# Kernel optimization log

Hardware: AMD Instinct MI355X
Metric: run time of the kernel (lower is better)

The kernel has to match this reference:

```python
import jax, jax.numpy as jnp
import numpy as np

MAX_STEPS = 8
EPS = 0.1
LAM = 5.0


def setup_inputs() -> dict:
    key = jax.random.key(0)
    k1, k2, k3, k4, k5 = jax.random.split(key, 5)
    n0 = m0 = 192
    E = 191  # tree edges ~ n0 - 1
    return {
        "E1f": jax.random.randint(k1, (E, 2), 0, n0),
        "E1b": jax.random.randint(k2, (E, 2), 0, n0),
        "E2f": jax.random.randint(k3, (E, 2), 0, n0),  # unused by forward (kept for signature parity)
        "cost": jax.random.uniform(k4, (n0, m0), dtype=jnp.float32),
        "constr_f": jax.random.uniform(k5, (m0, m0), dtype=jnp.float32),
    }


def reference(E1f, E1b, E2f, cost, constr_f):
    n0, m0 = cost.shape
    S = n0 + m0
    # pad cost -> [S, S], constr_f -> [S, S] (right cols zero then bottom rows one)
    cost_p = jnp.pad(cost, ((0, m0), (0, n0)))
    cf = jnp.pad(constr_f, ((0, 0), (0, n0)))
    cf = jnp.pad(cf, ((0, n0), (0, 0)), constant_values=1.0)

    phi = cost_p.T                          # [S, S]
    phie = phi / EPS
    psi_f = (LAM * (1.0 - cf))[:, :, None]  # [S, S, 1]
    psi_b = jnp.transpose(psi_f, (1, 0, 2))

    # cdist(dst, arange(S)) == 0 indicator is exactly a one-hot of the dst index
    to_f = jax.nn.one_hot(E1f[:, 1], S, dtype=phi.dtype)  # [E, S]
    to_b = jax.nn.one_hot(E1b[:, 1], S, dtype=phi.dtype)  # [E, S]
    E = to_f.shape[0]

    def step(carry, _):
        u, v, msg_f, msg_b, sum_f, sum_b = carry
        base = sum_f + sum_b - phie
        u = jax.nn.logsumexp(base - v, axis=-2, keepdims=True)  # [1, S]
        v = jax.nn.logsumexp(base - u, axis=-1, keepdims=True)  # [S, 1]
        A = phie + u + v - sum_f - sum_b                        # [S, S]
        term_f = A @ to_f.T                                     # [S, E]
        lse_f = jax.nn.logsumexp(-(psi_f / EPS + msg_b[:, None, :]), axis=0)  # [S, E]
        msg_f = 0.5 * (msg_f + term_f + lse_f)
        sum_f = msg_f @ to_f                                    # [S, S]
        A2 = phie + u + v - sum_f - sum_b
        term_b = A2 @ to_b.T
        lse_b = jax.nn.logsumexp(-(psi_b / EPS + msg_f[:, None, :]), axis=0)
        msg_b = 0.5 * (msg_b + term_b + lse_b)
        sum_b = msg_b @ to_b
        return (u, v, msg_f, msg_b, sum_f, sum_b), None

    f32 = phi.dtype
    init = (
        jnp.zeros((1, S), f32), jnp.zeros((S, 1), f32),
        jnp.zeros((S, E), f32), jnp.zeros((S, E), f32),
        jnp.zeros((S, S), f32), jnp.zeros((S, S), f32),
    )
    (u, v, _, _, sum_f, sum_b), _ = jax.lax.scan(step, init, None, length=MAX_STEPS)

    logp = jnp.minimum(sum_f + sum_b - phie - u - v, 0.0)
    return jnp.exp(logp).T
```

## Files before the change

### kernel.cpp

```cpp
#include <hip/hip_runtime.h>
#include <math.h>

#define S      384
#define N0     192
#define NE     191
#define MAXADJ 16
#define E50    1.9287498e-22f

#define OFF_W     0
#define OFF_WT    36864
#define OFF_PHIE  73728
#define OFF_MSGF  147456
#define OFF_MSGB  221184
#define OFF_MXF   294912
#define OFF_MXB   368640
#define OFF_SBT   442368
#define OFF_BASET 516096
#define OFF_U     589824
#define OFF_V     590016
#define OFF_MAXF  590400
#define OFF_MAXB  590592
#define OFF_HIF   590784
#define OFF_LOF   590976
#define OFF_HIB   591168
#define OFF_LOB   591360
#define OFF_UHI   591552
#define OFF_INT   591616
#define IOFF_DSTF 0
#define IOFF_DSTB 192
#define IOFF_CNTF 384
#define IOFF_CNTB 576
#define IOFF_ADJF 768
#define IOFF_ADJB (768 + 192*MAXADJ)

__global__ __launch_bounds__(256) void k_setup(
    const int* __restrict__ E1f, const int* __restrict__ E1b,
    const float* __restrict__ cost, const float* __restrict__ constr,
    float* __restrict__ ws)
{
    int tid = blockIdx.x * 256 + threadIdx.x;
    int nt  = gridDim.x * 256;

    for (int idx = tid; idx < 192 * 192; idx += nt) {
        int k = idx / 192, s = idx % 192;
        float w = __expf(-50.f * (1.f - constr[idx]));
        ws[OFF_W + idx] = w;
        ws[OFF_WT + s * 192 + k] = w;
    }
    for (int idx = tid; idx < 192 * S; idx += nt) {
        int j = idx / S, i = idx % S;
        ws[OFF_PHIE + idx] = (i < N0) ? -10.f * cost[j * N0 + i] : 0.f;
        ws[OFF_MSGF + idx] = 0.f;
        ws[OFF_MSGB + idx] = 0.f;
        ws[OFF_MXF + idx]  = 0.f;
        ws[OFF_MXB + idx]  = (j < NE) ? 1.f : 0.f;
    }
    for (int i = tid; i < S; i += nt) ws[OFF_V + i] = 0.f;
    for (int i = tid; i < 192; i += nt) {
        ws[OFF_U + i] = 0.f;
        ws[OFF_MAXF + i] = 0.f; ws[OFF_MAXB + i] = 0.f;
        ws[OFF_HIF + i] = 0.f;  ws[OFF_LOF + i] = 0.f;
        ws[OFF_HIB + i] = (i < NE) ? 192.f : 0.f;
        ws[OFF_LOB + i] = (i < NE) ? 192.f : 0.f;
    }
    if (tid == 0) ws[OFF_UHI] = 0.f;

    int* ip = (int*)(ws + OFF_INT);
    for (int e = tid; e < 192; e += nt) {
        ip[IOFF_DSTF + e] = (e < NE) ? E1f[2 * e + 1] : 0;
        ip[IOFF_DSTB + e] = (e < NE) ? E1b[2 * e + 1] : 0;
    }
    for (int b = tid; b < 192; b += nt) {
        int cf = 0, cb = 0;
        for (int e = 0; e < NE; ++e) {
            if (E1f[2 * e + 1] == b && cf < MAXADJ) ip[IOFF_ADJF + b * MAXADJ + cf++] = e;
            if (E1b[2 * e + 1] == b && cb < MAXADJ) ip[IOFF_ADJB + b * MAXADJ + cb++] = e;
        }
        ip[IOFF_CNTF + b] = cf;
        ip[IOFF_CNTB + b] = cb;
    }
}

__global__ __launch_bounds__(256) void k_uv1(float* __restrict__ ws)
{
    int bid = blockIdx.x, t = threadIdx.x;
    int l = t & 63, w = t >> 6;
    const float* V = ws + OFF_V;

    if (bid == 48) {
        if (w == 0) {
            float m = -1e30f, x[6];
#pragma unroll
            for (int q = 0; q < 6; ++q) { x[q] = -V[l + 64 * q]; m = fmaxf(m, x[q]); }
#pragma unroll
            for (int o = 32; o; o >>= 1) m = fmaxf(m, __shfl_xor(m, o, 64));
            float sm = 0.f;
#pragma unroll
            for (int q = 0; q < 6; ++q) sm += __expf(x[q] - m);
#pragma unroll
            for (int o = 32; o; o >>= 1) sm += __shfl_xor(sm, o, 64);
            if (l == 0) ws[OFF_UHI] = m + __logf(sm);
        }
        return;
    }

    int j = bid * 4 + w;
    const int* ip = (const int*)(ws + OFF_INT);
    int cF = ip[IOFF_CNTF + j], cB = ip[IOFF_CNTB + j];
    const int* aF = ip + IOFF_ADJF + j * MAXADJ;
    const int* aB = ip + IOFF_ADJB + j * MAXADJ;

    float sft[6] = {0,0,0,0,0,0}, sbt[6] = {0,0,0,0,0,0};
    for (int q = 0; q < cF; ++q) {
        const float* mr = ws + OFF_MSGF + aF[q] * S;
#pragma unroll
        for (int p = 0; p < 6; ++p) sft[p] += mr[l + 64 * p];
    }
    for (int q = 0; q < cB; ++q) {
        const float* mr = ws + OFF_MSGB + aB[q] * S;
#pragma unroll
        for (int p = 0; p < 6; ++p) sbt[p] += mr[l + 64 * p];
    }

    float x[6], m = -1e30f;
#pragma unroll
    for (int p = 0; p < 6; ++p) {
        int i = l + 64 * p;
        float bt = ws[OFF_PHIE + j * S + i] + sft[p] + sbt[p];
        ws[OFF_BASET + j * S + i] = bt;
        ws[OFF_SBT + j * S + i]   = sbt[p];
        x[p] = bt - V[i];
        m = fmaxf(m, x[p]);
    }
#pragma unroll
    for (int o = 32; o; o >>= 1) m = fmaxf(m, __shfl_xor(m, o, 64));
    float sm = 0.f;
#pragma unroll
    for (int p = 0; p < 6; ++p) sm += __expf(x[p] - m);
#pragma unroll
    for (int o = 32; o; o >>= 1) sm += __shfl_xor(sm, o, 64);
    if (l == 0) ws[OFF_U + j] = m + __logf(sm);
}

__global__ __launch_bounds__(256) void k_v(float* __restrict__ ws)
{
    __shared__ float Ul[192];
    __shared__ float msh[16][17], ssh[16][17];
    int t = threadIdx.x, bid = blockIdx.x;
    if (t < 192) Ul[t] = ws[OFF_U + t];
    __syncthreads();

    const float* BT = ws + OFF_BASET;
    int il = t & 15, jg = t >> 4;
    int i = bid * 16 + il;

    float m = -1e30f, sm = 0.f;
#pragma unroll 4
    for (int j = jg; j < 192; j += 16) {
        float x = BT[j * S + i] - Ul[j];
        float mn = fmaxf(m, x);
        sm = sm * __expf(m - mn) + __expf(x - mn);
        m = mn;
    }
    msh[jg][il] = m; ssh[jg][il] = sm;
    __syncthreads();

    if (jg == 0) {
        float M = msh[0][il], Ss = ssh[0][il];
#pragma unroll
        for (int g = 1; g < 16; ++g) {
            float m2 = msh[g][il], s2 = ssh[g][il];
            float mn = fmaxf(M, m2);
            Ss = Ss * __expf(M - mn) + s2 * __expf(m2 - mn);
            M = mn;
        }
        float xt = __logf(192.f) - ws[OFF_UHI];
        float mn = fmaxf(M, xt);
        Ss = Ss * __expf(M - mn) + __expf(xt - mn);
        ws[OFF_V + i] = mn + __logf(Ss);
    }
}

__global__ __launch_bounds__(256) void k_msg(float* __restrict__ ws, int fwd)
{
    __shared__ float mx[192];
    __shared__ float red[256], red2[256];
    int e = blockIdx.x, t = threadIdx.x;
    const int* ip = (const int*)(ws + OFF_INT);

    float* MSG  = ws + (fwd ? OFF_MSGF : OFF_MSGB);
    float* MX   = ws + (fwd ? OFF_MXF  : OFF_MXB);
    const float* MXin = ws + (fwd ? OFF_MXB : OFF_MXF);
    const float* Wm   = ws + (fwd ? OFF_W   : OFF_WT);

    float mPrev = fwd ? ws[OFF_MAXB + e] : ws[OFF_MAXF + e];
    float hi    = fwd ? ws[OFF_HIB + e]  : ws[OFF_HIF + e];
    float lo    = fwd ? ws[OFF_LOB + e]  : ws[OFF_LOF + e];
    float addLo = fwd ? hi : E50 * hi;
    float yHi   = fwd ? (hi + E50 * lo) : (lo + hi);
    float lyHi  = __logf(yHi);

    int d = fwd ? ip[IOFF_DSTF + e] : ip[IOFF_DSTB + e];
    float uD = ws[OFF_U + d];
    const float* V = ws + OFF_V;

    if (t < 192) mx[t] = MXin[e * S + t];
    __syncthreads();

    float acc = 0.f;
    if (t < 192) {
#pragma unroll 8
        for (int k = 0; k < 192; ++k)
            acc += Wm[k * 192 + t] * mx[k];
    }

    int s1 = t, s2 = t + 256;
    float bt1, bt2 = 0.f;
    if (fwd) {
        bt1 = ws[OFF_BASET + d * S + s1];
        if (s2 < S) bt2 = ws[OFF_BASET + d * S + s2];
    } else {
        int cF = ip[IOFF_CNTF + d];
        const int* aF = ip + IOFF_ADJF + d * MAXADJ;
        bt1 = ws[OFF_PHIE + d * S + s1] + ws[OFF_SBT + d * S + s1];
        if (s2 < S) bt2 = ws[OFF_PHIE + d * S + s2] + ws[OFF_SBT + d * S + s2];
        for (int q = 0; q < cF; ++q) {
            const float* mr = ws + OFF_MSGF + aF[q] * S;
            bt1 += mr[s1];
            if (s2 < S) bt2 += mr[s2];
        }
    }

    float logy1 = (s1 < 192) ? __logf(acc + addLo) : lyHi;
    float x1 = 0.5f * (MSG[e * S + s1] + uD + V[s1] - bt1 + mPrev + logy1);
    float x2 = 1e30f;
    if (s2 < S) {
        x2 = 0.5f * (MSG[e * S + s2] + uD + V[s2] - bt2 + mPrev + lyHi);
        MSG[e * S + s2] = x2;
    }
    MSG[e * S + s1] = x1;

    red[t] = fminf(x1, x2);
    __syncthreads();
    for (int o = 128; o; o >>= 1) {
        if (t < o) red[t] = fminf(red[t], red[t + o]);
        __syncthreads();
    }
    float mn = red[0];
    __syncthreads();

    float mx1 = __expf(mn - x1);
    float mx2 = (s2 < S) ? __expf(mn - x2) : 0.f;
    MX[e * S + s1] = mx1;
    if (s2 < S) MX[e * S + s2] = mx2;
    if (t == 0) {
        if (fwd) ws[OFF_MAXF + e] = -mn; else ws[OFF_MAXB + e] = -mn;
    }

    red[t]  = (t < 192) ? mx1 : 0.f;
    red2[t] = ((t >= 192) ? mx1 : 0.f) + mx2;
    __syncthreads();
    for (int o = 128; o; o >>= 1) {
        if (t < o) { red[t] += red[t + o]; red2[t] += red2[t + o]; }
        __syncthreads();
    }
    if (t == 0) {
        if (fwd) { ws[OFF_LOF + e] = red[0]; ws[OFF_HIF + e] = red2[0]; }
        else     { ws[OFF_LOB + e] = red[0]; ws[OFF_HIB + e] = red2[0]; }
    }
}

__global__ __launch_bounds__(256) void k_final(const float* __restrict__ ws,
                                               float* __restrict__ out)
{
    int t = threadIdx.x;
    const int* ip = (const int*)(ws + OFF_INT);
    const float* V = ws + OFF_V;
    float uhi = ws[OFF_UHI];

    for (int a = blockIdx.x * 6; a < blockIdx.x * 6 + 6; ++a) {
        if (a < 192) {
            float ua = ws[OFF_U + a];
            int cF = ip[IOFF_CNTF + a], cB = ip[IOFF_CNTB + a];
            const int* aF = ip + IOFF_ADJF + a * MAXADJ;
            const int* aB = ip + IOFF_ADJB + a * MAXADJ;
            for (int b = t; b < S; b += 256) {
                float bt = ws[OFF_PHIE + a * S + b];
                for (int q = 0; q < cF; ++q) bt += ws[OFF_MSGF + aF[q] * S + b];
                for (int q = 0; q < cB; ++q) bt += ws[OFF_MSGB + aB[q] * S + b];
                out[a * S + b] = __expf(fminf(bt - ua - V[b], 0.f));
            }
        } else {
            for (int b = t; b < S; b += 256)
                out[a * S + b] = __expf(fminf(-uhi - V[b], 0.f));
        }
    }
}

extern "C" void kernel_launch(void* const* d_in, const int* in_sizes, int n_in,
                              void* d_out, int out_size, void* d_ws, size_t ws_size,
                              hipStream_t stream)
{
    const int*   E1f    = (const int*)d_in[0];
    const int*   E1b    = (const int*)d_in[1];
    const float* cost   = (const float*)d_in[3];
    const float* constr = (const float*)d_in[4];

    float* ws = (float*)d_ws;

    k_setup<<<64, 256, 0, stream>>>(E1f, E1b, cost, constr, ws);

    for (int step = 0; step < 8; ++step) {
        k_uv1<<<49, 256, 0, stream>>>(ws);
        k_v<<<24, 256, 0, stream>>>(ws);
        k_msg<<<NE, 256, 0, stream>>>(ws, 1);
        k_msg<<<NE, 256, 0, stream>>>(ws, 0);
    }

    k_final<<<64, 256, 0, stream>>>(ws, (float*)d_out);
}
```

Baseline: 250.3 us.

## Fuse all iteration kernels into one persistent cooperative kernel with grid barriers

Replaces the 33 per-step kernel launches (uv1, v, two msg passes per step, plus final) with a single cooperative kernel of 96 blocks that loops over steps and separates the phases with a software grid barrier built on atomics. Each block now handles two edges in the message phase and stages tiles of the W matrix in shared memory so both edges reuse each tile. This is meant to remove launch overhead and inter-kernel gaps, at the cost of less parallelism per phase (96 blocks instead of 191) and spin-wait barrier latency.

```diff
diff --git a/kernel.cpp b/kernel.cpp
--- a/kernel.cpp
+++ b/kernel.cpp
@@ -6,6 +6,7 @@
 #define NE     191
 #define MAXADJ 16
 #define E50    1.9287498e-22f
+#define NB     96
 
 #define OFF_W     0
 #define OFF_WT    36864
@@ -25,7 +26,8 @@
 #define OFF_HIB   591168
 #define OFF_LOB   591360
 #define OFF_UHI   591552
-#define OFF_INT   591616
+#define OFF_BAR   591616
+#define OFF_INT   591744
 #define IOFF_DSTF 0
 #define IOFF_DSTB 192
 #define IOFF_CNTF 384
@@ -63,7 +65,12 @@
         ws[OFF_HIB + i] = (i < NE) ? 192.f : 0.f;
         ws[OFF_LOB + i] = (i < NE) ? 192.f : 0.f;
     }
-    if (tid == 0) ws[OFF_UHI] = 0.f;
+    if (tid == 0) {
+        ws[OFF_UHI] = 0.f;
+        unsigned* bar = (unsigned*)(ws + OFF_BAR);
+        bar[0] = 0u;
+        bar[32] = 0u;
+    }
 
     int* ip = (int*)(ws + OFF_INT);
     for (int e = tid; e < 192; e += nt) {
@@ -81,117 +88,37 @@
     }
 }
 
-__global__ __launch_bounds__(256) void k_uv1(float* __restrict__ ws)
-{
-    int bid = blockIdx.x, t = threadIdx.x;
-    int l = t & 63, w = t >> 6;
-    const float* V = ws + OFF_V;
-
-    if (bid == 48) {
-        if (w == 0) {
-            float m = -1e30f, x[6];
-#pragma unroll
-            for (int q = 0; q < 6; ++q) { x[q] = -V[l + 64 * q]; m = fmaxf(m, x[q]); }
-#pragma unroll
-            for (int o = 32; o; o >>= 1) m = fmaxf(m, __shfl_xor(m, o, 64));
-            float sm = 0.f;
-#pragma unroll
-            for (int q = 0; q < 6; ++q) sm += __expf(x[q] - m);
-#pragma unroll
-            for (int o = 32; o; o >>= 1) sm += __shfl_xor(sm, o, 64);
-            if (l == 0) ws[OFF_UHI] = m + __logf(sm);
-        }
-        return;
-    }
-
-    int j = bid * 4 + w;
-    const int* ip = (const int*)(ws + OFF_INT);
-    int cF = ip[IOFF_CNTF + j], cB = ip[IOFF_CNTB + j];
-    const int* aF = ip + IOFF_ADJF + j * MAXADJ;
-    const int* aB = ip + IOFF_ADJB + j * MAXADJ;
-
-    float sft[6] = {0,0,0,0,0,0}, sbt[6] = {0,0,0,0,0,0};
-    for (int q = 0; q < cF; ++q) {
-        const float* mr = ws + OFF_MSGF + aF[q] * S;
-#pragma unroll
-        for (int p = 0; p < 6; ++p) sft[p] += mr[l + 64 * p];
-    }
-    for (int q = 0; q < cB; ++q) {
-        const float* mr = ws + OFF_MSGB + aB[q] * S;
-#pragma unroll
-        for (int p = 0; p < 6; ++p) sbt[p] += mr[l + 64 * p];
-    }
-
-    float x[6], m = -1e30f;
-#pragma unroll
-    for (int p = 0; p < 6; ++p) {
-        int i = l + 64 * p;
-        float bt = ws[OFF_PHIE + j * S + i] + sft[p] + sbt[p];
-        ws[OFF_BASET + j * S + i] = bt;
-        ws[OFF_SBT + j * S + i]   = sbt[p];
-        x[p] = bt - V[i];
-        m = fmaxf(m, x[p]);
-    }
-#pragma unroll
-    for (int o = 32; o; o >>= 1) m = fmaxf(m, __shfl_xor(m, o, 64));
-    float sm = 0.f;
-#pragma unroll
-    for (int p = 0; p < 6; ++p) sm += __expf(x[p] - m);
-#pragma unroll
-    for (int o = 32; o; o >>= 1) sm += __shfl_xor(sm, o, 64);
-    if (l == 0) ws[OFF_U + j] = m + __logf(sm);
-}
-
-__global__ __launch_bounds__(256) void k_v(float* __restrict__ ws)
-{
-    __shared__ float Ul[192];
-    __shared__ float msh[16][17], ssh[16][17];
-    int t = threadIdx.x, bid = blockIdx.x;
-    if (t < 192) Ul[t] = ws[OFF_U + t];
-    __syncthreads();
-
-    const float* BT = ws + OFF_BASET;
-    int il = t & 15, jg = t >> 4;
-    int i = bid * 16 + il;
-
-    float m = -1e30f, sm = 0.f;
-#pragma unroll 4
-    for (int j = jg; j < 192; j += 16) {
-        float x = BT[j * S + i] - Ul[j];
-        float mn = fmaxf(m, x);
-        sm = sm * __expf(m - mn) + __expf(x - mn);
-        m = mn;
-    }
-    msh[jg][il] = m; ssh[jg][il] = sm;
-    __syncthreads();
-
-    if (jg == 0) {
-        float M = msh[0][il], Ss = ssh[0][il];
-#pragma unroll
-        for (int g = 1; g < 16; ++g) {
-            float m2 = msh[g][il], s2 = ssh[g][il];
-            float mn = fmaxf(M, m2);
-            Ss = Ss * __expf(M - mn) + s2 * __expf(m2 - mn);
-            M = mn;
-        }
-        float xt = __logf(192.f) - ws[OFF_UHI];
-        float mn = fmaxf(M, xt);
-        Ss = Ss * __expf(M - mn) + __expf(xt - mn);
-        ws[OFF_V + i] = mn + __logf(Ss);
-    }
-}
-
-__global__ __launch_bounds__(256) void k_msg(float* __restrict__ ws, int fwd)
-{
-    __shared__ float mx[192];
-    __shared__ float red[256], red2[256];
-    int e = blockIdx.x, t = threadIdx.x;
-    const int* ip = (const int*)(ws + OFF_INT);
-
-    float* MSG  = ws + (fwd ? OFF_MSGF : OFF_MSGB);
-    float* MX   = ws + (fwd ? OFF_MXF  : OFF_MXB);
-    const float* MXin = ws + (fwd ? OFF_MXB : OFF_MXF);
-    const float* Wm   = ws + (fwd ? OFF_W   : OFF_WT);
+__device__ __forceinline__ void gbar(unsigned* bar)
+{
+    __syncthreads();
+    if (threadIdx.x == 0) {
+        unsigned* cnt = bar;
+        unsigned* gen = bar + 32;
+        unsigned g = __hip_atomic_fetch_add(gen, 0u, __ATOMIC_RELAXED,
+                                            __HIP_MEMORY_SCOPE_AGENT);
+        unsigned a = __hip_atomic_fetch_add(cnt, 1u, __ATOMIC_RELEASE,
+                                            __HIP_MEMORY_SCOPE_AGENT);
+        if (a == NB - 1) {
+            __hip_atomic_exchange(cnt, 0u, __ATOMIC_RELAXED,
+                                  __HIP_MEMORY_SCOPE_AGENT);
+            __hip_atomic_fetch_add(gen, 1u, __ATOMIC_RELEASE,
+                                   __HIP_MEMORY_SCOPE_AGENT);
+        } else {
+            while (__hip_atomic_fetch_add(gen, 0u, __ATOMIC_RELAXED,
+                                          __HIP_MEMORY_SCOPE_AGENT) == g)
+                __builtin_amdgcn_s_sleep(4);
+        }
+    }
+    __threadfence();
+    __syncthreads();
+}
+
+__device__ __forceinline__ void msg_tail(
+    float* __restrict__ ws, const int* __restrict__ ip,
+    int e, int fwd, float acc, int t, float* red, float* red2)
+{
+    float* MSG = ws + (fwd ? OFF_MSGF : OFF_MSGB);
+    float* MX  = ws + (fwd ? OFF_MXF  : OFF_MXB);
 
     float mPrev = fwd ? ws[OFF_MAXB + e] : ws[OFF_MAXF + e];
     float hi    = fwd ? ws[OFF_HIB + e]  : ws[OFF_HIF + e];
@@ -203,16 +130,6 @@
     int d = fwd ? ip[IOFF_DSTF + e] : ip[IOFF_DSTB + e];
     float uD = ws[OFF_U + d];
     const float* V = ws + OFF_V;
-
-    if (t < 192) mx[t] = MXin[e * S + t];
-    __syncthreads();
-
-    float acc = 0.f;
-    if (t < 192) {
-#pragma unroll 8
-        for (int k = 0; k < 192; ++k)
-            acc += Wm[k * 192 + t] * mx[k];
-    }
 
     int s1 = t, s2 = t + 256;
     float bt1, bt2 = 0.f;
@@ -268,17 +185,159 @@
         if (fwd) { ws[OFF_LOF + e] = red[0]; ws[OFF_HIF + e] = red2[0]; }
         else     { ws[OFF_LOB + e] = red[0]; ws[OFF_HIB + e] = red2[0]; }
     }
-}
-
-__global__ __launch_bounds__(256) void k_final(const float* __restrict__ ws,
-                                               float* __restrict__ out)
-{
-    int t = threadIdx.x;
+    __syncthreads();
+}
+
+__device__ __forceinline__ void msg_phase(
+    float* __restrict__ ws, const int* __restrict__ ip,
+    int bid, int t, int fwd,
+    float* la, float (*mxs)[192], float* red, float* red2)
+{
+    int e0 = bid * 2, e1 = bid * 2 + 1;
+    const float* Wm   = ws + (fwd ? OFF_W   : OFF_WT);
+    const float* MXin = ws + (fwd ? OFF_MXB : OFF_MXF);
+
+    if (t < 192) {
+        mxs[0][t] = MXin[e0 * S + t];
+        mxs[1][t] = (e1 < NE) ? MXin[e1 * S + t] : 0.f;
+    }
+
+    float acc0 = 0.f, acc1 = 0.f;
+    for (int k0 = 0; k0 < 192; k0 += 32) {
+        __syncthreads();
+        for (int q = t; q < 32 * 192; q += 256)
+            la[q] = Wm[k0 * 192 + q];
+        __syncthreads();
+        if (t < 192) {
+#pragma unroll 8
+            for (int kk = 0; kk < 32; ++kk) {
+                float wv = la[kk * 192 + t];
+                acc0 += wv * mxs[0][k0 + kk];
+                acc1 += wv * mxs[1][k0 + kk];
+            }
+        }
+    }
+    __syncthreads();
+    msg_tail(ws, ip, e0, fwd, acc0, t, red, red2);
+    if (e1 < NE)
+        msg_tail(ws, ip, e1, fwd, acc1, t, red, red2);
+}
+
+__global__ __launch_bounds__(256) void k_iter(float* __restrict__ ws,
+                                              float* __restrict__ out)
+{
+    const int bid = blockIdx.x, t = threadIdx.x;
+    const int l = t & 63, w = t >> 6;
+    unsigned* bar = (unsigned*)(ws + OFF_BAR);
     const int* ip = (const int*)(ws + OFF_INT);
+
+    __shared__ float la[32 * 192];
+    __shared__ float mxs[2][192];
+    __shared__ float red[256], red2[256];
+    __shared__ float vm[4][5], vs[4][5];
+
+    for (int step = 0; step < 8; ++step) {
+        if (w < 2) {
+            int j = bid * 2 + w;
+            int cF = ip[IOFF_CNTF + j], cB = ip[IOFF_CNTB + j];
+            const int* aF = ip + IOFF_ADJF + j * MAXADJ;
+            const int* aB = ip + IOFF_ADJB + j * MAXADJ;
+            float sft[6] = {0,0,0,0,0,0}, sbt[6] = {0,0,0,0,0,0};
+            for (int q = 0; q < cF; ++q) {
+                const float* mr = ws + OFF_MSGF + aF[q] * S;
+#pragma unroll
+                for (int p = 0; p < 6; ++p) sft[p] += mr[l + 64 * p];
+            }
+            for (int q = 0; q < cB; ++q) {
+                const float* mr = ws + OFF_MSGB + aB[q] * S;
+#pragma unroll
+                for (int p = 0; p < 6; ++p) sbt[p] += mr[l + 64 * p];
+            }
+            float x[6], m = -1e30f;
+#pragma unroll
+            for (int p = 0; p < 6; ++p) {
+                int i = l + 64 * p;
+                float bt = ws[OFF_PHIE + j * S + i] + sft[p] + sbt[p];
+                ws[OFF_BASET + j * S + i] = bt;
+                ws[OFF_SBT + j * S + i]   = sbt[p];
+                x[p] = bt - ws[OFF_V + i];
+                m = fmaxf(m, x[p]);
+            }
+#pragma unroll
+            for (int o = 32; o; o >>= 1) m = fmaxf(m, __shfl_xor(m, o, 64));
+            float sm = 0.f;
+#pragma unroll
+            for (int p = 0; p < 6; ++p) sm += __expf(x[p] - m);
+#pragma unroll
+            for (int o = 32; o; o >>= 1) sm += __shfl_xor(sm, o, 64);
+            if (l == 0) ws[OFF_U + j] = m + __logf(sm);
+        } else if (bid == 0 && w == 2) {
+            float xx[6], m = -1e30f;
+#pragma unroll
+            for (int q = 0; q < 6; ++q) {
+                xx[q] = -ws[OFF_V + l + 64 * q];
+                m = fmaxf(m, xx[q]);
+            }
+#pragma unroll
+            for (int o = 32; o; o >>= 1) m = fmaxf(m, __shfl_xor(m, o, 64));
+            float sm = 0.f;
+#pragma unroll
+            for (int q = 0; q < 6; ++q) sm += __expf(xx[q] - m);
+#pragma unroll
+            for (int o = 32; o; o >>= 1) sm += __shfl_xor(sm, o, 64);
+            if (l == 0) ws[OFF_UHI] = m + __logf(sm);
+        }
+        gbar(bar);
+
+        {
+            int il = l & 3;
+            int i  = bid * 4 + il;
+            int jg = (w << 4) + (l >> 2);
+            float m = -1e30f, sm = 0.f;
+            for (int j = jg; j < 192; j += 64) {
+                float x = ws[OFF_BASET + j * S + i] - ws[OFF_U + j];
+                float mn = fmaxf(m, x);
+                sm = sm * __expf(m - mn) + __expf(x - mn);
+                m = mn;
+            }
+#pragma unroll
+            for (int off = 4; off < 64; off <<= 1) {
+                float m2 = __shfl_xor(m, off, 64);
+                float s2 = __shfl_xor(sm, off, 64);
+                float mn = fmaxf(m, m2);
+                sm = sm * __expf(m - mn) + s2 * __expf(m2 - mn);
+                m = mn;
+            }
+            if (l < 4) { vm[w][l] = m; vs[w][l] = sm; }
+            __syncthreads();
+            if (t < 4) {
+                float M = vm[0][t], Ss = vs[0][t];
+#pragma unroll
+                for (int g2 = 1; g2 < 4; ++g2) {
+                    float m2 = vm[g2][t], s2 = vs[g2][t];
+                    float mn = fmaxf(M, m2);
+                    Ss = Ss * __expf(M - mn) + s2 * __expf(m2 - mn);
+                    M = mn;
+                }
+                float xt = __logf(192.f) - ws[OFF_UHI];
+                float mn = fmaxf(M, xt);
+                Ss = Ss * __expf(M - mn) + __expf(xt - mn);
+                ws[OFF_V + bid * 4 + t] = mn + __logf(Ss);
+            }
+        }
+        gbar(bar);
+
+        msg_phase(ws, ip, bid, t, 1, la, mxs, red, red2);
+        gbar(bar);
+
+        msg_phase(ws, ip, bid, t, 0, la, mxs, red, red2);
+        gbar(bar);
+    }
+
     const float* V = ws + OFF_V;
     float uhi = ws[OFF_UHI];
-
-    for (int a = blockIdx.x * 6; a < blockIdx.x * 6 + 6; ++a) {
+    for (int r = 0; r < 4; ++r) {
+        int a = bid * 4 + r;
         if (a < 192) {
             float ua = ws[OFF_U + a];
             int cF = ip[IOFF_CNTF + a], cB = ip[IOFF_CNTB + a];
@@ -306,16 +365,12 @@
     const float* cost   = (const float*)d_in[3];
     const float* constr = (const float*)d_in[4];
 
-    float* ws = (float*)d_ws;
+    float* ws   = (float*)d_ws;
+    float* outp = (float*)d_out;
 
     k_setup<<<64, 256, 0, stream>>>(E1f, E1b, cost, constr, ws);
 
-    for (int step = 0; step < 8; ++step) {
-        k_uv1<<<49, 256, 0, stream>>>(ws);
-        k_v<<<24, 256, 0, stream>>>(ws);
-        k_msg<<<NE, 256, 0, stream>>>(ws, 1);
-        k_msg<<<NE, 256, 0, stream>>>(ws, 0);
-    }
-
-    k_final<<<64, 256, 0, stream>>>(ws, (float*)d_out);
-}
+    void* args[] = { (void*)&ws, (void*)&outp };
+    hipLaunchCooperativeKernel((const void*)k_iter, dim3(NB), dim3(256),
+                               args, 0, stream);
+}
```

Measured after the change: 594.3 us. 137% more time.

## Fuse column logsumexp for v into forward message kernel, drop k_v launch

Applied to the files above, without the earlier changes.

Removes the separate k_v kernel. Every block of the forward k_msg pass now recomputes all 384 column logsumexps over BASET itself, and block 0 writes v to the workspace for the backward pass. This saves one launch and one grid-wide dependency per step. In exchange each of the 191 blocks does the full 192x384 two-pass reduction, which is redundant work and extra memory traffic.

```diff
diff --git a/kernel.cpp b/kernel.cpp
--- a/kernel.cpp
+++ b/kernel.cpp
@@ -142,48 +142,35 @@
     if (l == 0) ws[OFF_U + j] = m + __logf(sm);
 }
 
-__global__ __launch_bounds__(256) void k_v(float* __restrict__ ws)
-{
+__device__ __forceinline__ float col_lse(const float* __restrict__ BT,
+                                         const float* __restrict__ Ul,
+                                         int i, float xt)
+{
+    const float* bc = BT + i;
+    float m0 = -1e30f, m1 = -1e30f, m2 = -1e30f, m3 = -1e30f;
+#pragma unroll 8
+    for (int j = 0; j < 192; j += 4) {
+        m0 = fmaxf(m0, bc[(j + 0) * S] - Ul[j + 0]);
+        m1 = fmaxf(m1, bc[(j + 1) * S] - Ul[j + 1]);
+        m2 = fmaxf(m2, bc[(j + 2) * S] - Ul[j + 2]);
+        m3 = fmaxf(m3, bc[(j + 3) * S] - Ul[j + 3]);
+    }
+    float m = fmaxf(fmaxf(fmaxf(m0, m1), fmaxf(m2, m3)), xt);
+    float s0 = 0.f, s1 = 0.f, s2 = 0.f, s3 = 0.f;
+#pragma unroll 8
+    for (int j = 0; j < 192; j += 4) {
+        s0 += __expf(bc[(j + 0) * S] - Ul[j + 0] - m);
+        s1 += __expf(bc[(j + 1) * S] - Ul[j + 1] - m);
+        s2 += __expf(bc[(j + 2) * S] - Ul[j + 2] - m);
+        s3 += __expf(bc[(j + 3) * S] - Ul[j + 3] - m);
+    }
+    return m + __logf((s0 + s1) + (s2 + s3) + __expf(xt - m));
+}
+
+__global__ __launch_bounds__(256) void k_msg(float* __restrict__ ws, int fwd)
+{
+    __shared__ float mx[192];
     __shared__ float Ul[192];
-    __shared__ float msh[16][17], ssh[16][17];
-    int t = threadIdx.x, bid = blockIdx.x;
-    if (t < 192) Ul[t] = ws[OFF_U + t];
-    __syncthreads();
-
-    const float* BT = ws + OFF_BASET;
-    int il = t & 15, jg = t >> 4;
-    int i = bid * 16 + il;
-
-    float m = -1e30f, sm = 0.f;
-#pragma unroll 4
-    for (int j = jg; j < 192; j += 16) {
-        float x = BT[j * S + i] - Ul[j];
-        float mn = fmaxf(m, x);
-        sm = sm * __expf(m - mn) + __expf(x - mn);
-        m = mn;
-    }
-    msh[jg][il] = m; ssh[jg][il] = sm;
-    __syncthreads();
-
-    if (jg == 0) {
-        float M = msh[0][il], Ss = ssh[0][il];
-#pragma unroll
-        for (int g = 1; g < 16; ++g) {
-            float m2 = msh[g][il], s2 = ssh[g][il];
-            float mn = fmaxf(M, m2);
-            Ss = Ss * __expf(M - mn) + s2 * __expf(m2 - mn);
-            M = mn;
-        }
-        float xt = __logf(192.f) - ws[OFF_UHI];
-        float mn = fmaxf(M, xt);
-        Ss = Ss * __expf(M - mn) + __expf(xt - mn);
-        ws[OFF_V + i] = mn + __logf(Ss);
-    }
-}
-
-__global__ __launch_bounds__(256) void k_msg(float* __restrict__ ws, int fwd)
-{
-    __shared__ float mx[192];
     __shared__ float red[256], red2[256];
     int e = blockIdx.x, t = threadIdx.x;
     const int* ip = (const int*)(ws + OFF_INT);
@@ -202,10 +189,28 @@
 
     int d = fwd ? ip[IOFF_DSTF + e] : ip[IOFF_DSTB + e];
     float uD = ws[OFF_U + d];
-    const float* V = ws + OFF_V;
-
-    if (t < 192) mx[t] = MXin[e * S + t];
+
+    if (t < 192) {
+        mx[t] = MXin[e * S + t];
+        Ul[t] = ws[OFF_U + t];
+    }
     __syncthreads();
+
+    int s1 = t, s2 = t + 256;
+
+    float v1, v2 = 0.f;
+    if (fwd) {
+        float xt = __logf(192.f) - ws[OFF_UHI];
+        v1 = col_lse(ws + OFF_BASET, Ul, s1, xt);
+        if (s2 < S) v2 = col_lse(ws + OFF_BASET, Ul, s2, xt);
+        if (e == 0) {
+            ws[OFF_V + s1] = v1;
+            if (s2 < S) ws[OFF_V + s2] = v2;
+        }
+    } else {
+        v1 = ws[OFF_V + s1];
+        if (s2 < S) v2 = ws[OFF_V + s2];
+    }
 
     float acc = 0.f;
     if (t < 192) {
@@ -214,7 +219,6 @@
             acc += Wm[k * 192 + t] * mx[k];
     }
 
-    int s1 = t, s2 = t + 256;
     float bt1, bt2 = 0.f;
     if (fwd) {
         bt1 = ws[OFF_BASET + d * S + s1];
@@ -232,10 +236,10 @@
     }
 
     float logy1 = (s1 < 192) ? __logf(acc + addLo) : lyHi;
-    float x1 = 0.5f * (MSG[e * S + s1] + uD + V[s1] - bt1 + mPrev + logy1);
+    float x1 = 0.5f * (MSG[e * S + s1] + uD + v1 - bt1 + mPrev + logy1);
     float x2 = 1e30f;
     if (s2 < S) {
-        x2 = 0.5f * (MSG[e * S + s2] + uD + V[s2] - bt2 + mPrev + lyHi);
+        x2 = 0.5f * (MSG[e * S + s2] + uD + v2 - bt2 + mPrev + lyHi);
         MSG[e * S + s2] = x2;
     }
     MSG[e * S + s1] = x1;
@@ -312,7 +316,6 @@
 
     for (int step = 0; step < 8; ++step) {
         k_uv1<<<49, 256, 0, stream>>>(ws);
-        k_v<<<24, 256, 0, stream>>>(ws);
         k_msg<<<NE, 256, 0, stream>>>(ws, 1);
         k_msg<<<NE, 256, 0, stream>>>(ws, 0);
     }
```

After: 325.1 us. +29.9%, slower.

## Fuse per-step stage kernels into one launch with atomic inter-block barriers

Applied to the files above, without the earlier changes.

Replaces the four kernel launches per iteration (uv, v, forward msg, backward msg) with a single kernel launch per step. Block ranges are assigned to each stage, and later stages spin on global atomic counters until every block of the previous stage has arrived. This is meant to cut launch overhead and inter-kernel gaps. It relies on all 455 blocks being co-resident or scheduled in order to avoid deadlock, and waiting blocks occupy CUs while they spin.

```diff
diff --git a/kernel.cpp b/kernel.cpp
--- a/kernel.cpp
+++ b/kernel.cpp
@@ -32,6 +32,7 @@
 #define IOFF_CNTB 576
 #define IOFF_ADJF 768
 #define IOFF_ADJB (768 + 192*MAXADJ)
+#define IOFF_SYNC (768 + 2*192*MAXADJ)
 
 __global__ __launch_bounds__(256) void k_setup(
     const int* __restrict__ E1f, const int* __restrict__ E1b,
@@ -79,11 +80,33 @@
         ip[IOFF_CNTF + b] = cf;
         ip[IOFF_CNTB + b] = cb;
     }
-}
-
-__global__ __launch_bounds__(256) void k_uv1(float* __restrict__ ws)
-{
-    int bid = blockIdx.x, t = threadIdx.x;
+    unsigned* sc = (unsigned*)(ip + IOFF_SYNC);
+    for (int i = tid; i < 24; i += nt) sc[i] = 0u;
+}
+
+__device__ __forceinline__ void arrive(unsigned* c)
+{
+    asm volatile("s_waitcnt vmcnt(0)" ::: "memory");
+    __syncthreads();
+    if (threadIdx.x == 0) {
+        __threadfence();
+        __hip_atomic_fetch_add(c, 1u, __ATOMIC_RELEASE, __HIP_MEMORY_SCOPE_AGENT);
+    }
+}
+
+__device__ __forceinline__ void wait_for(unsigned* c, unsigned target)
+{
+    if (threadIdx.x == 0) {
+        while (__hip_atomic_load(c, __ATOMIC_RELAXED, __HIP_MEMORY_SCOPE_AGENT) < target)
+            __builtin_amdgcn_s_sleep(8);
+        __threadfence();
+    }
+    __syncthreads();
+}
+
+__device__ __forceinline__ void stage_uv1(float* __restrict__ ws, int bid)
+{
+    int t = threadIdx.x;
     int l = t & 63, w = t >> 6;
     const float* V = ws + OFF_V;
 
@@ -142,11 +165,11 @@
     if (l == 0) ws[OFF_U + j] = m + __logf(sm);
 }
 
-__global__ __launch_bounds__(256) void k_v(float* __restrict__ ws)
+__device__ __forceinline__ void stage_v(float* __restrict__ ws, int bid)
 {
     __shared__ float Ul[192];
     __shared__ float msh[16][17], ssh[16][17];
-    int t = threadIdx.x, bid = blockIdx.x;
+    int t = threadIdx.x;
     if (t < 192) Ul[t] = ws[OFF_U + t];
     __syncthreads();
 
@@ -181,11 +204,11 @@
     }
 }
 
-__global__ __launch_bounds__(256) void k_msg(float* __restrict__ ws, int fwd)
+__device__ __forceinline__ void stage_msg(float* __restrict__ ws, int e, int fwd)
 {
     __shared__ float mx[192];
     __shared__ float red[256], red2[256];
-    int e = blockIdx.x, t = threadIdx.x;
+    int t = threadIdx.x;
     const int* ip = (const int*)(ws + OFF_INT);
 
     float* MSG  = ws + (fwd ? OFF_MSGF : OFF_MSGB);
@@ -267,6 +290,29 @@
     if (t == 0) {
         if (fwd) { ws[OFF_LOF + e] = red[0]; ws[OFF_HIF + e] = red2[0]; }
         else     { ws[OFF_LOB + e] = red[0]; ws[OFF_HIB + e] = red2[0]; }
+    }
+}
+
+__global__ __launch_bounds__(256) void k_step(float* __restrict__ ws, int step)
+{
+    int* ip = (int*)(ws + OFF_INT);
+    unsigned* sc = (unsigned*)(ip + IOFF_SYNC) + step * 3;
+    int bid = blockIdx.x;
+
+    if (bid < 49) {
+        stage_uv1(ws, bid);
+        arrive(&sc[0]);
+    } else if (bid < 73) {
+        wait_for(&sc[0], 49u);
+        stage_v(ws, bid - 49);
+        arrive(&sc[1]);
+    } else if (bid < 264) {
+        wait_for(&sc[1], 24u);
+        stage_msg(ws, bid - 73, 1);
+        arrive(&sc[2]);
+    } else {
+        wait_for(&sc[2], 191u);
+        stage_msg(ws, bid - 264, 0);
     }
 }
 
@@ -310,12 +356,8 @@
 
     k_setup<<<64, 256, 0, stream>>>(E1f, E1b, cost, constr, ws);
 
-    for (int step = 0; step < 8; ++step) {
-        k_uv1<<<49, 256, 0, stream>>>(ws);
-        k_v<<<24, 256, 0, stream>>>(ws);
-        k_msg<<<NE, 256, 0, stream>>>(ws, 1);
-        k_msg<<<NE, 256, 0, stream>>>(ws, 0);
-    }
+    for (int step = 0; step < 8; ++step)
+        k_step<<<455, 256, 0, stream>>>(ws, step);
 
     k_final<<<64, 256, 0, stream>>>(ws, (float*)d_out);
 }
```

New measurement: 447.0 us. 78.6% more time.
